# Kernel tuning notes

Measured on AMD Instinct MI355X. Metric: run time of the kernel, lower is better.

Reference implementation:

```python
import jax, jax.numpy as jnp
import numpy as np

R_CUT = 10.0  # init arg r_cut


def _per_mol(pos, T, eneg, node_attrs, an, q_tot, eidx, hardness, cov_radii):
    # pos [N,3], T [N,E], eneg [N], node_attrs [N,num_el], an [N] int,
    # q_tot scalar, eidx [2,E] int
    N = pos.shape[0]
    E = T.shape[1]
    dtype = pos.dtype
    sqrt_pi = jnp.sqrt(jnp.pi).astype(dtype)
    sqrt_2 = jnp.sqrt(2.0).astype(dtype)
    eye = jnp.eye(N, dtype=dtype)
    # pairwise distances; +eye makes the (masked-out) diagonal sqrt-safe
    diff = pos[:, None, :] - pos[None, :, :]
    d = jnp.sqrt(jnp.sum(diff * diff, axis=-1) + eye)  # [N,N]
    r = cov_radii[an]                                   # [N]
    sigma = r * r
    gamma = jnp.sqrt(sigma[:, None] + sigma[None, :])   # [N,N]
    diag_vals = hardness[jnp.argmax(node_attrs, axis=-1)] + 1.0 / (sqrt_pi * r)
    A = jax.scipy.special.erf(d / (sqrt_2 * gamma)) / d * (1.0 - eye) + jnp.diag(diag_vals)
    # per-edge cutoff diagonal: 1/cos(pi*r/(2*r_cut)) - 1
    e0, e1 = eidx[0], eidx[1]
    edge_d = jnp.sqrt(jnp.sum((pos[e0] - pos[e1]) ** 2, axis=-1))  # [E]
    cut = 1.0 / jnp.cos(jnp.pi * edge_d / (2.0 * R_CUT)) - 1.0
    Ap = T.T @ A @ T + jnp.diag(cut)                    # [E,E]
    # augment with charge-conservation row/col of ones
    ones_col = jnp.ones((E, 1), dtype=dtype)
    ones_row = jnp.ones((1, E + 1), dtype=dtype)
    Aaug = jnp.concatenate([jnp.concatenate([Ap, ones_col], axis=1), ones_row], axis=0)
    b = jnp.concatenate([-(T.T @ eneg), q_tot[None]])   # [E+1]
    x = jnp.linalg.solve(Aaug, b)[:-1]                  # [E] split charges
    return T @ x                                        # [N] atomic partial charges


def setup_inputs() -> dict:
    key = jax.random.key(0)
    B, N, E, NUM_EL, NZ = 256, 64, 512, 10, 119
    ks = jax.random.split(key, 10)
    positions = jax.random.normal(ks[0], (B, N, 3), dtype=jnp.float32)
    T = jax.random.normal(ks[1], (B, N, E), dtype=jnp.float32)
    eneg = jax.random.normal(ks[2], (B, N), dtype=jnp.float32)
    node_attrs = jax.random.normal(ks[3], (B, N, NUM_EL), dtype=jnp.float32)
    total_charge = jax.random.normal(ks[4], (B,), dtype=jnp.float32)
    atomic_numbers = jax.random.randint(ks[5], (B, N), 1, 100)
    e0 = jax.random.randint(ks[6], (B, E), 0, N)
    off = jax.random.randint(ks[7], (B, E), 1, N)
    edge_index = jnp.stack([e0, (e0 + off) % N], axis=1)  # [B,2,E], distinct endpoints
    hardness = jax.random.uniform(ks[8], (NUM_EL,), dtype=jnp.float32)
    cov_radii = 0.3 + 2.2 * jax.random.uniform(ks[9], (NZ,), dtype=jnp.float32)
    p = jnp.zeros((1,), dtype=jnp.float32)  # only used for .device in torch
    return dict(positions=positions, T=T, eneg=eneg, node_attrs=node_attrs,
                total_charge=total_charge, p=p, hardness=hardness,
                cov_radii=cov_radii, atomic_numbers=atomic_numbers,
                edge_index=edge_index)


def reference(positions, T, eneg, node_attrs, total_charge, p, hardness,
              cov_radii, atomic_numbers, edge_index):
    charges = jax.vmap(_per_mol, in_axes=(0, 0, 0, 0, 0, 0, 0, None, None))(
        positions, T, eneg, node_attrs, atomic_numbers, total_charge,
        edge_index, hardness, cov_radii)  # [B,N]
    return charges.reshape(-1)  # concat over molecules, as in the torch loop
```

## Files before the change

kernel.cpp:

```cpp
#include <hip/hip_runtime.h>
#include <math.h>

#define SQRT_PI 1.7724538509055160273
#define SQRT_2  1.4142135623730950488
#define PI_OVER_2RC 0.15707963267948966

typedef double dbl4 __attribute__((ext_vector_type(4)));


__device__ __forceinline__ double bcast64(double v, int lane) {
    union { double d; unsigned int u[2]; } a, r;
    a.d = v;
    r.u[0] = __builtin_amdgcn_readlane(a.u[0], lane);
    r.u[1] = __builtin_amdgcn_readlane(a.u[1], lane);
    return r.d;
}

__device__ __forceinline__ double a_entry(int i, int j, const double* posd,
                                          const double* sig, const double* dg) {
    if (i == j) return dg[i];
    double dx = posd[3*i+0]-posd[3*j+0];
    double dy = posd[3*i+1]-posd[3*j+1];
    double dz = posd[3*i+2]-posd[3*j+2];
    double d  = sqrt(dx*dx+dy*dy+dz*dz);
    double g  = sqrt(sig[i]+sig[j]);
    return erf(d/(SQRT_2*g))/d;
}

__device__ __forceinline__ dbl4 mfma64(int cS, double xv, double yv, dbl4 acc) {
    return cS ? __builtin_amdgcn_mfma_f64_16x16x4f64(yv, xv, acc, 0, 0, 0)
              : __builtin_amdgcn_mfma_f64_16x16x4f64(xv, yv, acc, 0, 0, 0);
}

__global__ __launch_bounds__(64)
void k0_probe(double* __restrict__ fl)
{
    const int l = threadIdx.x;
    const int kl = l >> 4, ml = l & 15;
    const double af1 = (double)(l + 1),  bf1 = (double)(l + 65);
    const double af2 = (double)(1 + ((l*7 + 3) % 61));
    const double bf2 = (double)(2 + ((l*13 + 5) % 53));
    dbl4 c1 = {0.0,0.0,0.0,0.0}, c2 = {0.0,0.0,0.0,0.0};
    c1 = __builtin_amdgcn_mfma_f64_16x16x4f64(af1, bf1, c1, 0, 0, 0);
    c2 = __builtin_amdgcn_mfma_f64_16x16x4f64(af2, bf2, c2, 0, 0, 0);
    int best = -1;
    for (int h = 0; h < 32; ++h) {
        if (best >= 0) break;
        const int cS = h >> 4, cA = (h >> 3) & 1, cB = (h >> 2) & 1, cD = h & 3;
        bool ok = true;
        #pragma unroll
        for (int r = 0; r < 4; ++r) {
            int row, col;
            const int v0 = 4*kl + r, v1 = kl + 4*r;
            if (cD == 0)      { row = v0; col = ml; }
            else if (cD == 1) { row = v1; col = ml; }
            else if (cD == 2) { row = ml; col = v0; }
            else              { row = ml; col = v1; }
            double r1 = 0.0, r2 = 0.0;
            #pragma unroll
            for (int k = 0; k < 4; ++k) {
                const int la = cA ? (row*4 + k) : (row + 16*k);
                const int lb = cB ? (col*4 + k) : (col + 16*k);
                if (cS == 0) {
                    r1 += (double)(la + 1) * (double)(lb + 65);
                    r2 += (double)(1 + ((la*7+3) % 61)) * (double)(2 + ((lb*13+5) % 53));
                } else {
                    r1 += (double)(lb + 1) * (double)(la + 65);
                    r2 += (double)(1 + ((lb*7+3) % 61)) * (double)(2 + ((la*13+5) % 53));
                }
            }
            if (c1[r] != r1 || c2[r] != r2) ok = false;
        }
        if (__ballot(ok) == ~0ull) best = h;
    }
    if (l == 0) {
        fl[0] = (best >= 0) ? 1.0 : 0.0;
        fl[1] = (double)((best >= 0) ? (best >> 4)      : 0);
        fl[2] = (double)((best >= 0) ? ((best >> 3) & 1) : 0);
        fl[3] = (double)((best >= 0) ? ((best >> 2) & 1) : 0);
        fl[4] = (double)((best >= 0) ? (best & 3)        : 0);
    }
}

__global__ __launch_bounds__(1024)
void k_fused(const float* __restrict__ pos, const float* __restrict__ T,
             const int* __restrict__ eidx, const float* __restrict__ nattr,
             const float* __restrict__ eneg, const float* __restrict__ qtot,
             const float* __restrict__ hard, const float* __restrict__ covr,
             const int* __restrict__ an, const double* __restrict__ flq,
             float* __restrict__ outp)
{
    const int m = blockIdx.x, tid = threadIdx.x;
    const int jl = tid & 63;
    const int rg = tid >> 6;
    const int kl = jl >> 4, ml = jl & 15;

    __shared__ double R[2*64*66];
    __shared__ double AB[64*65];
    __shared__ double w_sl[512];
    __shared__ double posd[192], sig_s[64], dg_s[64], eneg_s[64];
    __shared__ double t0a_s[64], t0b_s[64], ga_s[64], gb_s[64];
    __shared__ double ua_s[64], ub_s[64], sa_s[64], sb_s[64];
    __shared__ double dinv_s[64], dvec_s[64];
    __shared__ double lam_sh, sw_sh;

    double* const Ta = R;
    double* const Tb = R + 64*66;
    double* const SB = R;
    double* const Pm = R + 64*66;

    const int cS = (int)flq[1], cA = (int)flq[2], cB = (int)flq[3], cD = (int)flq[4];
    const int aRow = cA ? (jl >> 2) : ml;
    const int aK   = cA ? (jl & 3)  : kl;
    const int bRow = cB ? (jl >> 2) : ml;
    const int bK   = cB ? (jl & 3)  : kl;
    int drow[4], dcol[4];
    #pragma unroll
    for (int r = 0; r < 4; ++r) {
        const int v0 = 4*kl + r, v1 = kl + 4*r;
        if (cD == 0)      { drow[r] = v0; dcol[r] = ml; }
        else if (cD == 1) { drow[r] = v1; dcol[r] = ml; }
        else if (cD == 2) { drow[r] = ml; dcol[r] = v0; }
        else              { drow[r] = ml; dcol[r] = v1; }
    }

    const float* Tm = T + (size_t)m*64*512;
    const int srow = tid >> 4, sc4 = (tid & 15) * 4;

    float4 v = *(const float4*)&Tm[srow*512 + sc4];

    if (tid < 64) {
        posd[3*tid+0] = (double)pos[(m*64+tid)*3+0];
        posd[3*tid+1] = (double)pos[(m*64+tid)*3+1];
        posd[3*tid+2] = (double)pos[(m*64+tid)*3+2];
        double r = (double)covr[an[m*64+tid]];
        sig_s[tid] = r*r;
        const float* np_ = nattr + (size_t)(m*64+tid)*10;
        float best = np_[0]; int bi = 0;
        #pragma unroll
        for (int k = 1; k < 10; ++k) { float vv = np_[k]; if (vv > best) { best = vv; bi = k; } }
        dg_s[tid] = (double)hard[bi] + 1.0/(SQRT_PI*r);
    } else if (tid < 128) {
        int ll = tid - 64;
        eneg_s[ll] = (double)eneg[m*64 + ll];
    }
    __syncthreads();

    if (tid < 512) {
        const int a0 = eidx[(size_t)m*1024 + tid];
        const int a1 = eidx[(size_t)m*1024 + 512 + tid];
        double dx = posd[3*a0+0]-posd[3*a1+0];
        double dy = posd[3*a0+1]-posd[3*a1+1];
        double dz = posd[3*a0+2]-posd[3*a1+2];
        double d  = sqrt(dx*dx+dy*dy+dz*dz);
        w_sl[tid] = 1.0 / (1.0/cos(PI_OVER_2RC*d) - 1.0);
    }

    int tp, tq, wm;
    switch (rg) {
        case 0:  tp=0; tq=0; wm=0; break;
        case 5:  tp=1; tq=1; wm=0; break;
        case 10: tp=2; tq=2; wm=0; break;
        case 15: tp=3; tq=3; wm=0; break;
        case 1:  tp=1; tq=0; wm=1; break;
        case 2:  tp=1; tq=0; wm=2; break;
        case 3:  tp=2; tq=0; wm=1; break;
        case 4:  tp=2; tq=0; wm=2; break;
        case 6:  tp=2; tq=1; wm=1; break;
        case 7:  tp=2; tq=1; wm=2; break;
        case 8:  tp=3; tq=0; wm=1; break;
        case 9:  tp=3; tq=0; wm=2; break;
        case 11: tp=3; tq=1; wm=1; break;
        case 12: tp=3; tq=1; wm=2; break;
        case 13: tp=3; tq=2; wm=1; break;
        default: tp=3; tq=2; wm=2; break;
    }
    const double* ta_b = &Ta[(size_t)(tp*16 + aRow)*66 + aK];
    const double* tb_b = &Tb[(size_t)(tq*16 + bRow)*66 + bK];
    dbl4 vacc = {0.0, 0.0, 0.0, 0.0};
    double t0b_p = 0.0;
    double areg[4];

    #pragma unroll
    for (int cc = 0; cc < 8; ++cc) {
        __syncthreads();
        const double w0 = w_sl[cc*64 + sc4+0];
        const double w1 = w_sl[cc*64 + sc4+1];
        const double w2 = w_sl[cc*64 + sc4+2];
        const double w3 = w_sl[cc*64 + sc4+3];
        const double d0 = (double)v.x, d1 = (double)v.y;
        const double d2 = (double)v.z, d3 = (double)v.w;
        {
            double2 p0; p0.x = d0; p0.y = d1;
            double2 p1; p1.x = d2; p1.y = d3;
            *(double2*)&Ta[srow*66 + sc4]     = p0;
            *(double2*)&Ta[srow*66 + sc4 + 2] = p1;
            double2 q0; q0.x = w0*d0; q0.y = w1*d1;
            double2 q1; q1.x = w2*d2; q1.y = w3*d3;
            *(double2*)&Tb[srow*66 + sc4]     = q0;
            *(double2*)&Tb[srow*66 + sc4 + 2] = q1;
        }
        t0b_p += d0*w0 + d1*w1 + d2*w2 + d3*w3;
        __syncthreads();
        if (cc < 7) v = *(const float4*)&Tm[srow*512 + (cc+1)*64 + sc4];
        if (cc == 0 && tid >= 128 && tid < 192) {
            const int ll = tid - 128;
            double s = 0.0;
            #pragma unroll
            for (int c = 0; c < 8; ++c) s += w_sl[c*64 + ll];
            #pragma unroll
            for (int off = 32; off > 0; off >>= 1) s += __shfl_down(s, off);
            if (ll == 0) sw_sh = s;
        }
        if (cc < 4) {
            const int i = rg + 16*cc;
            double av = a_entry(i, jl, posd, sig_s, dg_s);
            areg[cc] = av;
            AB[i*65 + jl] = av;
        }
        const bool act = (wm == 0) || (wm == 1 ? ((cc & 1) == 0) : ((cc & 1) == 1));
        if (act) {
            #pragma unroll
            for (int kk = 0; kk < 16; ++kk)
                vacc = mfma64(cS, ta_b[kk*4], tb_b[kk*4], vacc);
        }
    }
    __syncthreads();

    if (wm != 2) {
        #pragma unroll
        for (int r = 0; r < 4; ++r) {
            const int ri = tp*16 + drow[r], cj = tq*16 + dcol[r];
            SB[ri*66 + cj] = vacc[r];
            if (tp != tq) SB[cj*66 + ri] = vacc[r];
        }
    }
    {
        double t = t0b_p;
        t += __shfl_down(t, 8, 16);
        t += __shfl_down(t, 4, 16);
        t += __shfl_down(t, 2, 16);
        t += __shfl_down(t, 1, 16);
        if ((tid & 15) == 0) t0b_s[tid >> 4] = t;
    }
    __syncthreads();
    if (wm == 2) {
        #pragma unroll
        for (int r = 0; r < 4; ++r) {
            const int ri = tp*16 + drow[r], cj = tq*16 + dcol[r];
            const double vv = vacc[r];
            SB[ri*66 + cj] += vv;
            if (tp != tq) SB[cj*66 + ri] += vv;
        }
    }
    __syncthreads();

    {
        const int c16 = tid & 15, row16 = tid >> 4;
        double a = 0.0;
        #pragma unroll
        for (int kk = 0; kk < 4; ++kk)
            a += SB[row16*66 + 4*c16 + kk] * eneg_s[4*c16 + kk];
        a += __shfl_down(a, 8, 16);
        a += __shfl_down(a, 4, 16);
        a += __shfl_down(a, 2, 16);
        a += __shfl_down(a, 1, 16);
        if (c16 == 0) t0a_s[row16] = -a;
    }
    __syncthreads();

    {
        double ra[4], rb[4];
        const double ta = t0a_s[jl], tb = t0b_s[jl];
        #pragma unroll
        for (int p = 0; p < 4; ++p) { ra[p] = areg[p]*ta; rb[p] = areg[p]*tb; }
        #pragma unroll
        for (int off = 32; off > 0; off >>= 1) {
            #pragma unroll
            for (int p = 0; p < 4; ++p) {
                ra[p] += __shfl_down(ra[p], off);
                rb[p] += __shfl_down(rb[p], off);
            }
        }
        if (jl == 0) {
            #pragma unroll
            for (int p = 0; p < 4; ++p) { ga_s[rg+16*p] = ra[p]; gb_s[rg+16*p] = rb[p]; }
        }
    }
    __syncthreads();

    const int ti = rg >> 2, tj = rg & 3;
    {
        const double* xb = &AB[(size_t)(ti*16 + aRow)*65 + aK];
        const double* yb = &SB[(size_t)bK*66 + tj*16 + bRow];
        dbl4 pacc = {0.0, 0.0, 0.0, 0.0};
        #pragma unroll
        for (int kk = 0; kk < 16; ++kk)
            pacc = mfma64(cS, xb[kk*4], yb[kk*264], pacc);
        #pragma unroll
        for (int r = 0; r < 4; ++r)
            Pm[(ti*16 + drow[r])*66 + tj*16 + dcol[r]] = pacc[r];
    }
    __syncthreads();

    {
        dbl4 macc;
        #pragma unroll
        for (int r = 0; r < 4; ++r)
            macc[r] = AB[(ti*16 + drow[r])*65 + tj*16 + dcol[r]];
        const double* xb = &Pm[(size_t)(ti*16 + aRow)*66 + aK];
        const double* yb = &AB[(size_t)bK*65 + tj*16 + bRow];
        #pragma unroll
        for (int kk = 0; kk < 16; ++kk)
            macc = mfma64(cS, xb[kk*4], yb[kk*260], macc);
        __syncthreads();
        #pragma unroll
        for (int r = 0; r < 4; ++r)
            AB[(ti*16 + drow[r])*65 + tj*16 + dcol[r]] = macc[r];
    }
    __syncthreads();

    for (int pb = 0; pb < 4; ++pb) {
        const int kb = pb*16;
        if (tid < 64) {
            const int i = tid;
            double pr[16];
            #pragma unroll
            for (int c = 0; c < 16; ++c) pr[c] = AB[i*65 + kb + c];
            #pragma unroll
            for (int c = 0; c < 16; ++c) {
                const int k = kb + c;
                const double Dk = bcast64(pr[c], k);
                const double di = 1.0 / Dk;
                if (i == k) { dinv_s[k] = di; dvec_s[k] = Dk; }
                const double lik = pr[c] * di;
                #pragma unroll
                for (int j = c+1; j < 16; ++j) {
                    const double mkj = bcast64(pr[j], k);
                    if (i > k) pr[j] -= lik * mkj;
                }
                if (i > k) pr[c] = lik;
            }
            #pragma unroll
            for (int c = 0; c < 16; ++c) AB[i*65 + kb + c] = pr[c];
        }
        __syncthreads();
        const int lim = kb + 16;
        if (lim < 64) {
            double tacc[4] = {0.0, 0.0, 0.0, 0.0};
            #pragma unroll 4
            for (int c = 0; c < 16; ++c) {
                double lbv = AB[jl*65 + kb + c] * dvec_s[kb + c];
                #pragma unroll
                for (int p = 0; p < 4; ++p)
                    tacc[p] += AB[(rg+16*p)*65 + kb + c] * lbv;
            }
            if (jl >= lim) {
                #pragma unroll
                for (int p = 0; p < 4; ++p) {
                    int i = rg + 16*p;
                    if (i >= lim) AB[i*65 + jl] -= tacc[p];
                }
            }
        }
        __syncthreads();
    }

    if (tid < 128) {
        const int i = jl;
        double h = (rg == 0) ? ga_s[i] : gb_s[i];
        #pragma unroll
        for (int j = 0; j < 63; ++j) {
            double x = bcast64(h, j);
            double lij = (i > j) ? AB[i*65+j] : 0.0;
            h -= lij*x;
        }
        h *= dinv_s[i];
        #pragma unroll
        for (int j = 63; j > 0; --j) {
            double x = bcast64(h, j);
            double lji = (i < j) ? AB[j*65+i] : 0.0;
            h -= lji*x;
        }
        if (rg == 0) ua_s[i] = h; else ub_s[i] = h;
    }
    __syncthreads();

    {
        double ra[4], rb[4];
        const double uaj = ua_s[jl], ubj = ub_s[jl];
        #pragma unroll
        for (int p = 0; p < 4; ++p) { ra[p] = areg[p]*uaj; rb[p] = areg[p]*ubj; }
        #pragma unroll
        for (int off = 32; off > 0; off >>= 1) {
            #pragma unroll
            for (int p = 0; p < 4; ++p) {
                ra[p] += __shfl_down(ra[p], off);
                rb[p] += __shfl_down(rb[p], off);
            }
        }
        if (jl == 0) {
            #pragma unroll
            for (int p = 0; p < 4; ++p) {
                sa_s[rg + 16*p] = ra[p];
                sb_s[rg + 16*p] = rb[p];
            }
        }
    }
    __syncthreads();

    if (tid < 64) {
        double d1 = (eneg_s[tid] + sa_s[tid]) * t0b_s[tid];
        double d2 = sb_s[tid] * t0b_s[tid];
        #pragma unroll
        for (int off = 32; off > 0; off >>= 1) {
            d1 += __shfl_down(d1, off);
            d2 += __shfl_down(d2, off);
        }
        if (tid == 0) {
            double sY = -d1;
            double sZ = sw_sh - d2;
            lam_sh = ((double)qtot[m] - sY) / (1.0 - sZ);
        }
    }
    __syncthreads();
    if (tid < 64)
        outp[m*64 + tid] = (float)(ua_s[tid] - lam_sh*ub_s[tid]);
}

extern "C" void kernel_launch(void* const* d_in, const int* in_sizes, int n_in,
                              void* d_out, int out_size, void* d_ws, size_t ws_size,
                              hipStream_t stream) {
    const float* pos  = (const float*)d_in[0];
    const float* T    = (const float*)d_in[1];
    const float* eneg = (const float*)d_in[2];
    const float* nat  = (const float*)d_in[3];
    const float* qt   = (const float*)d_in[4];
    const float* hard = (const float*)d_in[6];
    const float* covr = (const float*)d_in[7];
    const int*   an   = (const int*)d_in[8];
    const int*   eidx = (const int*)d_in[9];
    float* outp = (float*)d_out;
    (void)n_in; (void)out_size; (void)ws_size;

    const int B = in_sizes[4];
    double* ws = (double*)d_ws;

    k0_probe<<<dim3(1), dim3(64), 0, stream>>>(ws);
    k_fused<<<dim3(B), dim3(1024), 0, stream>>>(pos, T, eidx, nat, eneg, qt,
                                                hard, covr, an, ws, outp);
}
```

Before: 162.6 us.

## Split MFMA accumulators, overlap reductions with GEMMs, drop final matvec via symmetry

```diff
diff --git a/kernel.cpp b/kernel.cpp
--- a/kernel.cpp
+++ b/kernel.cpp
@@ -100,7 +100,7 @@
     __shared__ double w_sl[512];
     __shared__ double posd[192], sig_s[64], dg_s[64], eneg_s[64];
     __shared__ double t0a_s[64], t0b_s[64], ga_s[64], gb_s[64];
-    __shared__ double ua_s[64], ub_s[64], sa_s[64], sb_s[64];
+    __shared__ double ua_s[64], ub_s[64];
     __shared__ double dinv_s[64], dvec_s[64];
     __shared__ double lam_sh, sw_sh;
 
@@ -177,7 +177,8 @@
     }
     const double* ta_b = &Ta[(size_t)(tp*16 + aRow)*66 + aK];
     const double* tb_b = &Tb[(size_t)(tq*16 + bRow)*66 + bK];
-    dbl4 vacc = {0.0, 0.0, 0.0, 0.0};
+    dbl4 vacc0 = {0.0, 0.0, 0.0, 0.0};
+    dbl4 vacc1 = {0.0, 0.0, 0.0, 0.0};
     double t0b_p = 0.0;
     double areg[4];
 
@@ -221,8 +222,10 @@
         const bool act = (wm == 0) || (wm == 1 ? ((cc & 1) == 0) : ((cc & 1) == 1));
         if (act) {
             #pragma unroll
-            for (int kk = 0; kk < 16; ++kk)
-                vacc = mfma64(cS, ta_b[kk*4], tb_b[kk*4], vacc);
+            for (int kk = 0; kk < 16; kk += 2) {
+                vacc0 = mfma64(cS, ta_b[kk*4],     tb_b[kk*4],     vacc0);
+                vacc1 = mfma64(cS, ta_b[(kk+1)*4], tb_b[(kk+1)*4], vacc1);
+            }
         }
     }
     __syncthreads();
@@ -231,8 +234,9 @@
         #pragma unroll
         for (int r = 0; r < 4; ++r) {
             const int ri = tp*16 + drow[r], cj = tq*16 + dcol[r];
-            SB[ri*66 + cj] = vacc[r];
-            if (tp != tq) SB[cj*66 + ri] = vacc[r];
+            const double vv = vacc0[r] + vacc1[r];
+            SB[ri*66 + cj] = vv;
+            if (tp != tq) SB[cj*66 + ri] = vv;
         }
     }
     {
@@ -248,43 +252,9 @@
         #pragma unroll
         for (int r = 0; r < 4; ++r) {
             const int ri = tp*16 + drow[r], cj = tq*16 + dcol[r];
-            const double vv = vacc[r];
+            const double vv = vacc0[r] + vacc1[r];
             SB[ri*66 + cj] += vv;
             if (tp != tq) SB[cj*66 + ri] += vv;
-        }
-    }
-    __syncthreads();
-
-    {
-        const int c16 = tid & 15, row16 = tid >> 4;
-        double a = 0.0;
-        #pragma unroll
-        for (int kk = 0; kk < 4; ++kk)
-            a += SB[row16*66 + 4*c16 + kk] * eneg_s[4*c16 + kk];
-        a += __shfl_down(a, 8, 16);
-        a += __shfl_down(a, 4, 16);
-        a += __shfl_down(a, 2, 16);
-        a += __shfl_down(a, 1, 16);
-        if (c16 == 0) t0a_s[row16] = -a;
-    }
-    __syncthreads();
-
-    {
-        double ra[4], rb[4];
-        const double ta = t0a_s[jl], tb = t0b_s[jl];
-        #pragma unroll
-        for (int p = 0; p < 4; ++p) { ra[p] = areg[p]*ta; rb[p] = areg[p]*tb; }
-        #pragma unroll
-        for (int off = 32; off > 0; off >>= 1) {
-            #pragma unroll
-            for (int p = 0; p < 4; ++p) {
-                ra[p] += __shfl_down(ra[p], off);
-                rb[p] += __shfl_down(rb[p], off);
-            }
-        }
-        if (jl == 0) {
-            #pragma unroll
-            for (int p = 0; p < 4; ++p) { ga_s[rg+16*p] = ra[p]; gb_s[rg+16*p] = rb[p]; }
         }
     }
     __syncthreads();
@@ -293,30 +263,66 @@
     {
         const double* xb = &AB[(size_t)(ti*16 + aRow)*65 + aK];
         const double* yb = &SB[(size_t)bK*66 + tj*16 + bRow];
-        dbl4 pacc = {0.0, 0.0, 0.0, 0.0};
-        #pragma unroll
-        for (int kk = 0; kk < 16; ++kk)
-            pacc = mfma64(cS, xb[kk*4], yb[kk*264], pacc);
+        dbl4 pacc0 = {0.0, 0.0, 0.0, 0.0};
+        dbl4 pacc1 = {0.0, 0.0, 0.0, 0.0};
+        #pragma unroll
+        for (int kk = 0; kk < 16; kk += 2) {
+            pacc0 = mfma64(cS, xb[kk*4],     yb[(size_t)kk*264],     pacc0);
+            pacc1 = mfma64(cS, xb[(kk+1)*4], yb[(size_t)(kk+1)*264], pacc1);
+        }
+        {
+            const int c16 = tid & 15, row16 = tid >> 4;
+            double a = 0.0;
+            #pragma unroll
+            for (int kk = 0; kk < 4; ++kk)
+                a += SB[row16*66 + 4*c16 + kk] * eneg_s[4*c16 + kk];
+            a += __shfl_down(a, 8, 16);
+            a += __shfl_down(a, 4, 16);
+            a += __shfl_down(a, 2, 16);
+            a += __shfl_down(a, 1, 16);
+            if (c16 == 0) t0a_s[row16] = -a;
+        }
         #pragma unroll
         for (int r = 0; r < 4; ++r)
-            Pm[(ti*16 + drow[r])*66 + tj*16 + dcol[r]] = pacc[r];
+            Pm[(ti*16 + drow[r])*66 + tj*16 + dcol[r]] = pacc0[r] + pacc1[r];
     }
     __syncthreads();
 
     {
-        dbl4 macc;
+        dbl4 macc0;
         #pragma unroll
         for (int r = 0; r < 4; ++r)
-            macc[r] = AB[(ti*16 + drow[r])*65 + tj*16 + dcol[r]];
+            macc0[r] = AB[(ti*16 + drow[r])*65 + tj*16 + dcol[r]];
+        dbl4 macc1 = {0.0, 0.0, 0.0, 0.0};
         const double* xb = &Pm[(size_t)(ti*16 + aRow)*66 + aK];
         const double* yb = &AB[(size_t)bK*65 + tj*16 + bRow];
         #pragma unroll
-        for (int kk = 0; kk < 16; ++kk)
-            macc = mfma64(cS, xb[kk*4], yb[kk*260], macc);
+        for (int kk = 0; kk < 16; kk += 2) {
+            macc0 = mfma64(cS, xb[kk*4],     yb[(size_t)kk*260],     macc0);
+            macc1 = mfma64(cS, xb[(kk+1)*4], yb[(size_t)(kk+1)*260], macc1);
+        }
+        {
+            double ra[4], rb[4];
+            const double ta = t0a_s[jl], tb = t0b_s[jl];
+            #pragma unroll
+            for (int p = 0; p < 4; ++p) { ra[p] = areg[p]*ta; rb[p] = areg[p]*tb; }
+            #pragma unroll
+            for (int off = 32; off > 0; off >>= 1) {
+                #pragma unroll
+                for (int p = 0; p < 4; ++p) {
+                    ra[p] += __shfl_down(ra[p], off);
+                    rb[p] += __shfl_down(rb[p], off);
+                }
+            }
+            if (jl == 0) {
+                #pragma unroll
+                for (int p = 0; p < 4; ++p) { ga_s[rg+16*p] = ra[p]; gb_s[rg+16*p] = rb[p]; }
+            }
+        }
         __syncthreads();
         #pragma unroll
         for (int r = 0; r < 4; ++r)
-            AB[(ti*16 + drow[r])*65 + tj*16 + dcol[r]] = macc[r];
+            AB[(ti*16 + drow[r])*65 + tj*16 + dcol[r]] = macc0[r] + macc1[r];
     }
     __syncthreads();
 
@@ -386,32 +392,10 @@
     }
     __syncthreads();
 
-    {
-        double ra[4], rb[4];
-        const double uaj = ua_s[jl], ubj = ub_s[jl];
-        #pragma unroll
-        for (int p = 0; p < 4; ++p) { ra[p] = areg[p]*uaj; rb[p] = areg[p]*ubj; }
-        #pragma unroll
-        for (int off = 32; off > 0; off >>= 1) {
-            #pragma unroll
-            for (int p = 0; p < 4; ++p) {
-                ra[p] += __shfl_down(ra[p], off);
-                rb[p] += __shfl_down(rb[p], off);
-            }
-        }
-        if (jl == 0) {
-            #pragma unroll
-            for (int p = 0; p < 4; ++p) {
-                sa_s[rg + 16*p] = ra[p];
-                sb_s[rg + 16*p] = rb[p];
-            }
-        }
-    }
-    __syncthreads();
-
     if (tid < 64) {
-        double d1 = (eneg_s[tid] + sa_s[tid]) * t0b_s[tid];
-        double d2 = sb_s[tid] * t0b_s[tid];
+        const double ua = ua_s[tid], ub = ub_s[tid], gbv = gb_s[tid];
+        double d1 = eneg_s[tid]*t0b_s[tid] + ua*gbv;
+        double d2 = ub*gbv;
         #pragma unroll
         for (int off = 32; off > 0; off >>= 1) {
             d1 += __shfl_down(d1, off);
```

After: 159.9 us. Within noise of the previous version (-1.7%).
